# Kernel optimization log

Measured on AMD Instinct MI355X. Metric: run time of the kernel, lower is better.

Reference implementation:

```python
import jax, jax.numpy as jnp
import numpy as np

DMODEL = 1024
NUM_HEADS = 16
HEAD_DIM = DMODEL // NUM_HEADS


def setup_inputs() -> dict:
    key = jax.random.key(0)
    k_x, k_wqkv, k_bqkv, k_wo, k_bo = jax.random.split(key, 5)
    B, T, D = 4, 2048, DMODEL
    s = 1.0 / np.sqrt(D)
    return {
        "x": jax.random.normal(k_x, (B, T, D), dtype=jnp.float32),
        "w_qkv": jax.random.uniform(k_wqkv, (D, 3 * D), dtype=jnp.float32, minval=-s, maxval=s),
        "b_qkv": jax.random.uniform(k_bqkv, (3 * D,), dtype=jnp.float32, minval=-s, maxval=s),
        "w_out": jax.random.uniform(k_wo, (D, D), dtype=jnp.float32, minval=-s, maxval=s),
        "b_out": jax.random.uniform(k_bo, (D,), dtype=jnp.float32, minval=-s, maxval=s),
    }


def reference(x, w_qkv, b_qkv, w_out, b_out):
    B, T, D = x.shape
    H, Hd = NUM_HEADS, HEAD_DIM
    qkv = x @ w_qkv + b_qkv                      # [B,T,3D]
    qkv = qkv.reshape(B, T, 3, H, Hd)
    q = jnp.transpose(qkv[:, :, 0], (0, 2, 1, 3))  # [B,H,T,Hd]
    k = jnp.transpose(qkv[:, :, 1], (0, 2, 1, 3))
    v = jnp.transpose(qkv[:, :, 2], (0, 2, 1, 3))
    scores = jnp.einsum("bhqd,bhkd->bhqk", q, k) / jnp.sqrt(jnp.float32(Hd))
    weights = jax.nn.softmax(scores, axis=-1)
    attn = jnp.einsum("bhqk,bhkd->bhqd", weights, v)  # [B,H,T,Hd]
    attn = jnp.transpose(attn, (0, 2, 1, 3)).reshape(B, T, D)
    return attn @ w_out + b_out
```

## Files before the change

### kernel.cpp

```cpp
#include <hip/hip_runtime.h>
#include <hip/hip_bf16.h>


typedef __bf16 bf16_t;
typedef __bf16 bf16x8 __attribute__((ext_vector_type(8)));
typedef float f32x4 __attribute__((ext_vector_type(4)));
typedef short short4v __attribute__((ext_vector_type(4)));

#if __has_builtin(__builtin_amdgcn_mfma_f32_16x16x16_bf16)
typedef __bf16 bf16x4 __attribute__((ext_vector_type(4)));
#define MFMA_PV(va, vb, c) __builtin_amdgcn_mfma_f32_16x16x16_bf16( \
    __builtin_bit_cast(bf16x4, (va)), __builtin_bit_cast(bf16x4, (vb)), (c), 0, 0, 0)
#else
#define MFMA_PV(va, vb, c) __builtin_amdgcn_mfma_f32_16x16x16bf16_1k((va), (vb), (c), 0, 0, 0)
#endif

#define DMODEL 1024
#define NH     16
#define HD     64
#define BATCH  4
#define SEQ    2048
#define NTOK   (BATCH * SEQ)
#define NOUT   (NTOK * DMODEL)
#define CEXP   0.1803368801111204f

__device__ __forceinline__ void async_ld16(void* lds, const void* g) {
  __builtin_amdgcn_global_load_lds(
      (const __attribute__((address_space(1))) void*)g,
      (__attribute__((address_space(3))) void*)lds, 16, 0, 0);
}

__global__ __launch_bounds__(256) void sniff_dtype(
    const uint4* __restrict__ x, int* __restrict__ flag) {
  int t = threadIdx.x;
  uint4 v = x[t];
  int nanish = 0, zc = 0;
  for (int j = 0; j < 4; ++j) {
    uint4 w = x[t + j * 256];
    unsigned u[4] = {w.x, w.y, w.z, w.w};
    for (int k = 0; k < 4; ++k) {
      unsigned lo = u[k] & 0xFFFFu, hi = u[k] >> 16;
      if ((lo & 0x7F80u) == 0x7F80u) nanish++;
      if ((hi & 0x7F80u) == 0x7F80u) nanish++;
      if (lo == 0) zc++;
      if (hi == 0) zc++;
    }
  }
  (void)v;
  __shared__ int rn[256], rz[256];
  rn[t] = nanish; rz[t] = zc;
  __syncthreads();
  for (int s = 128; s > 0; s >>= 1) {
    if (t < s) { rn[t] += rn[t + s]; rz[t] += rz[t + s]; }
    __syncthreads();
  }
  if (t == 0) flag[0] = (rn[0] > 4 || rz[0] > 2048) ? 1 : 0;
}

__global__ __launch_bounds__(256) void conv_to_bf16(
    const void* __restrict__ src, bf16_t* __restrict__ dst, int n,
    const int* __restrict__ flag) {
  int i = (blockIdx.x * 256 + threadIdx.x) * 8;
  if (i >= n) return;
  if (flag[0]) {
    const float4* s = (const float4*)((const float*)src + i);
    float4 a = s[0], b = s[1];
    bf16_t* o = dst + i;
    o[0] = (bf16_t)a.x; o[1] = (bf16_t)a.y; o[2] = (bf16_t)a.z; o[3] = (bf16_t)a.w;
    o[4] = (bf16_t)b.x; o[5] = (bf16_t)b.y; o[6] = (bf16_t)b.z; o[7] = (bf16_t)b.w;
  } else {
    *(uint4*)(dst + i) = *(const uint4*)((const bf16_t*)src + i);
  }
}

__global__ __launch_bounds__(256) void conv_biases(
    const void* __restrict__ sq, const void* __restrict__ so,
    float* __restrict__ dq, float* __restrict__ dofs,
    const int* __restrict__ flag) {
  int i = blockIdx.x * 256 + threadIdx.x;
  if (i < 3072)
    dq[i] = flag[0] ? ((const float*)sq)[i] : (float)((const bf16_t*)sq)[i];
  else {
    int j = i - 3072;
    dofs[j] = flag[0] ? ((const float*)so)[j] : (float)((const bf16_t*)so)[j];
  }
}

__global__ __launch_bounds__(256) void transpose_w(
    const void* __restrict__ in, bf16_t* __restrict__ out, int R, int C,
    const int* __restrict__ flag) {
  __shared__ bf16_t tile[32][33];
  const int tx = threadIdx.x & 31, ty = threadIdx.x >> 5;
  const int c0 = blockIdx.x * 32, r0 = blockIdx.y * 32;
  if (flag[0]) {
    for (int i = 0; i < 4; ++i) {
      int r = ty + i * 8;
      tile[r][tx] = (bf16_t)((const float*)in)[(size_t)(r0 + r) * C + c0 + tx];
    }
  } else {
    for (int i = 0; i < 4; ++i) {
      int r = ty + i * 8;
      tile[r][tx] = ((const bf16_t*)in)[(size_t)(r0 + r) * C + c0 + tx];
    }
  }
  __syncthreads();
  for (int i = 0; i < 4; ++i) {
    int r = ty + i * 8;
    out[(size_t)(c0 + r) * R + r0 + tx] = tile[tx][r];
  }
}

template <int MODE>
__global__ __launch_bounds__(256) void gemm_bt_bias(
    const bf16_t* __restrict__ A, const bf16_t* __restrict__ Bt,
    const float* __restrict__ bias, void* __restrict__ Cout,
    int M, int N, int K, const int* __restrict__ flag,
    bf16_t* __restrict__ vT) {
  __shared__ bf16_t sA[2][128 * 32];
  __shared__ bf16_t sB[2][128 * 32];
  const int t = threadIdx.x;
  const int wave = t >> 6, lane = t & 63;
  const int quad = lane >> 4, l16 = lane & 15;
  const int nwg = gridDim.x * gridDim.y;
  const int lin = blockIdx.y * gridDim.x + blockIdx.x;
  const int cpx = nwg >> 3;
  const int swz = (lin & 7) * cpx + (lin >> 3);
  const int bx = swz % gridDim.x, by = swz / gridDim.x;
  const int bM = by * 128, bN = bx * 128;
  const int m0w = (wave >> 1) * 64, n0w = (wave & 1) * 64;
  const int rowS = wave * 16 + (lane >> 2);
  const int kcS = (lane & 3) * 8;

  f32x4 acc[4][4] = {};

  auto stage = [&](int buf, int k0) {
    for (int r = 0; r < 2; ++r) {
      int row = r * 64 + rowS;
      async_ld16((char*)sA[buf] + r * 4096 + wave * 1024,
                 A + (size_t)(bM + row) * K + k0 + kcS);
      async_ld16((char*)sB[buf] + r * 4096 + wave * 1024,
                 Bt + (size_t)(bN + row) * K + k0 + kcS);
    }
  };

  const int nsteps = K >> 5;
  stage(0, 0);

  for (int s = 0; s < nsteps; ++s) {
    const int cur = s & 1;
    if (s + 1 < nsteps) {
      stage(cur ^ 1, (s + 1) << 5);
      asm volatile("s_waitcnt vmcnt(4)" ::: "memory");
    } else {
      asm volatile("s_waitcnt vmcnt(0)" ::: "memory");
    }
    __builtin_amdgcn_s_barrier();
    asm volatile("" ::: "memory");

    bf16x8 af[4], bfr[4];
    for (int i = 0; i < 4; ++i)
      af[i] = *(const bf16x8*)&sA[cur][(m0w + i * 16 + l16) * 32 + quad * 8];
    for (int j = 0; j < 4; ++j)
      bfr[j] = *(const bf16x8*)&sB[cur][(n0w + j * 16 + l16) * 32 + quad * 8];
    for (int i = 0; i < 4; ++i)
      for (int j = 0; j < 4; ++j)
        acc[i][j] = __builtin_amdgcn_mfma_f32_16x16x32_bf16(af[i], bfr[j], acc[i][j], 0, 0, 0);

    asm volatile("" ::: "memory");
    __builtin_amdgcn_s_barrier();
  }

  const bool f32out = (MODE == 1) && flag[0];
  for (int j = 0; j < 4; ++j) {
    int col = bN + n0w + j * 16 + l16;
    float bv = bias[col];
    for (int i = 0; i < 4; ++i) {
      int row0 = bM + m0w + i * 16 + quad * 4;
      if (MODE == 2 && col >= 2048) {
        int hh = (col - 2048) >> 6, dd = (col - 2048) & 63;
        bf16_t o4[4];
        for (int r = 0; r < 4; ++r) o4[r] = (bf16_t)(acc[i][j][r] + bv);
        size_t dst = ((((size_t)(row0 >> 11) * NH + hh) * HD + dd) << 11) | (row0 & 2047);
        *(uint2*)&vT[dst] = *(uint2*)o4;
      } else {
        float scale = (MODE == 2 && col < 1024) ? CEXP : 1.0f;
        for (int r = 0; r < 4; ++r) {
          float v = (acc[i][j][r] + bv) * scale;
          if (f32out) ((float*)Cout)[(size_t)(row0 + r) * N + col] = v;
          else        ((bf16_t*)Cout)[(size_t)(row0 + r) * N + col] = (bf16_t)v;
        }
      }
    }
  }
}

__global__ __launch_bounds__(512) void attention_v9(
    const bf16_t* __restrict__ qkv, const bf16_t* __restrict__ vT,
    bf16_t* __restrict__ attn) {
  const int t = threadIdx.x;
  const int wave = t >> 6, lane = t & 63;
  const int quad = lane >> 4, l16 = lane & 15;
  const int bh = blockIdx.x, b = bh >> 4, h = bh & 15;
  const int qw = blockIdx.y * 256 + wave * 32;

  __shared__ bf16_t Kt[2][128 * 64];
  __shared__ bf16_t Vt[2][64 * 128];

  const bf16_t* qglob = qkv + (size_t)b * SEQ * 3072 + h * 64;
  const bf16_t* kglob = qglob + 1024;
  const bf16_t* vglob = vT + (size_t)bh * HD * SEQ;

  bf16x8 qf[2][2];
  for (int s = 0; s < 2; ++s) {
    const bf16_t* qrow = qglob + (size_t)(qw + s * 16 + l16) * 3072 + quad * 8;
    qf[s][0] = *(const bf16x8*)qrow;
    qf[s][1] = *(const bf16x8*)(qrow + 32);
  }

  f32x4 accO[2][4] = {};
  f32x4 lp[2] = {};

  const int kRow = lane >> 3, kSlot = lane & 7;
  const int vRow = lane >> 4, vSlot = lane & 15;

  auto stageKV = [&](int buf, int kt) {
    for (int j = 0; j < 2; ++j) {
      int keyl = wave * 16 + j * 8 + kRow;
      int gc = kSlot ^ (keyl & 7);
      async_ld16((char*)Kt[buf] + (wave * 16 + j * 8) * 128,
                 kglob + (size_t)(kt + keyl) * 3072 + gc * 8);
    }
    for (int j = 0; j < 2; ++j) {
      int d = wave * 8 + j * 4 + vRow;
      int gc = vSlot ^ (d & 15);
      async_ld16((char*)Vt[buf] + (wave * 8 + j * 4) * 256,
                 vglob + (size_t)d * SEQ + kt + gc * 8);
    }
  };

  stageKV(0, 0);

  for (int ti = 0; ti < SEQ / 128; ++ti) {
    const int buf = ti & 1;
    __syncthreads();
    if (ti + 1 < SEQ / 128) stageKV(buf ^ 1, (ti + 1) * 128);

    const bf16_t* KtB = Kt[buf];
    const bf16_t* VtB = Vt[buf];

    for (int kb = 0; kb < 8; ++kb) {
      const bf16_t* kr = &KtB[(kb * 16 + l16) * 64];
      bf16x8 kf0 = *(const bf16x8*)(kr + ((quad ^ (l16 & 7)) * 8));
      bf16x8 kf1 = *(const bf16x8*)(kr + (((4 + quad) ^ (l16 & 7)) * 8));

      short4v pB[2];
      for (int s = 0; s < 2; ++s) {
        f32x4 z = {0.f, 0.f, 0.f, 0.f};
        f32x4 st = __builtin_amdgcn_mfma_f32_16x16x32_bf16(kf0, qf[s][0], z, 0, 0, 0);
        st = __builtin_amdgcn_mfma_f32_16x16x32_bf16(kf1, qf[s][1], st, 0, 0, 0);
        union { bf16_t hh[4]; short4v s4; } u;
        for (int r = 0; r < 4; ++r) {
          float p = __builtin_amdgcn_exp2f(st[r]);
          lp[s][r] += p;
          u.hh[r] = (bf16_t)p;
        }
        pB[s] = u.s4;
      }

      const int chunkbase = kb * 2 + (quad >> 1);
      const int coff = (quad & 1) * 4;
      for (int db = 0; db < 4; ++db) {
        short4v vf = *(const short4v*)&VtB[(db * 16 + l16) * 128 +
                                           ((chunkbase ^ l16) * 8) + coff];
        for (int s = 0; s < 2; ++s)
          accO[s][db] = MFMA_PV(vf, pB[s], accO[s][db]);
      }
    }
  }

  for (int s = 0; s < 2; ++s) {
    float l = (lp[s][0] + lp[s][1]) + (lp[s][2] + lp[s][3]);
    l += __shfl_xor(l, 16);
    l += __shfl_xor(l, 32);
    float inv = 1.f / l;
    size_t tok = (size_t)b * SEQ + qw + s * 16 + l16;
    for (int db = 0; db < 4; ++db) {
      bf16_t o4[4];
      for (int r = 0; r < 4; ++r) o4[r] = (bf16_t)(accO[s][db][r] * inv);
      *(uint2*)&attn[tok * DMODEL + h * HD + db * 16 + quad * 4] = *(uint2*)o4;
    }
  }
}

extern "C" void kernel_launch(void* const* d_in, const int* in_sizes, int n_in,
                              void* d_out, int out_size, void* d_ws, size_t ws_size,
                              hipStream_t stream) {
  const void* x     = d_in[0];
  const void* w_qkv = d_in[1];
  const void* b_qkv = d_in[2];
  const void* w_out = d_in[3];
  const void* b_out = d_in[4];

  char* ws = (char*)d_ws;
  int*    flag  = (int*)ws;
  bf16_t* wqkvT = (bf16_t*)(ws + 4096);
  bf16_t* woutT = (bf16_t*)(ws + 6295552);
  float*  bqkvf = (float*)(ws + 8392704);
  float*  boutf = (float*)(ws + 8404992);
  bf16_t* qkv   = (bf16_t*)(ws + 8409088);
  bf16_t* xb    = (bf16_t*)(ws + 58740736);
  bf16_t* attn  = xb;
  bf16_t* vTbuf = (bf16_t*)(ws + 75517952);

  sniff_dtype<<<1, 256, 0, stream>>>((const uint4*)x, flag);

  conv_to_bf16<<<NOUT / 2048, 256, 0, stream>>>(x, xb, NOUT, flag);
  conv_biases<<<16, 256, 0, stream>>>(b_qkv, b_out, bqkvf, boutf, flag);

  transpose_w<<<dim3(96, 32), 256, 0, stream>>>(w_qkv, wqkvT, 1024, 3072, flag);
  transpose_w<<<dim3(32, 32), 256, 0, stream>>>(w_out, woutT, 1024, 1024, flag);

  gemm_bt_bias<2><<<dim3(24, 64), 256, 0, stream>>>(
      xb, wqkvT, bqkvf, qkv, NTOK, 3072, 1024, flag, vTbuf);

  attention_v9<<<dim3(BATCH * NH, SEQ / 256), 512, 0, stream>>>(qkv, vTbuf, attn);

  gemm_bt_bias<1><<<dim3(8, 64), 256, 0, stream>>>(
      attn, woutT, boutf, d_out, NTOK, 1024, 1024, flag, nullptr);
}
```

Before: 302.2 us.

## Add 256x256-tile QKV GEMM kernel with swizzled LDS and interleaved staging

Replaces the 128x128 QKV projection GEMM with a new 512-thread kernel computing 256x256 tiles over K steps of 64. Each K step is split into halves whose async loads are interleaved with MFMA groups, with LDS offsets XOR-swizzled and wave priority raised around compute phases. The larger tile raises arithmetic intensity and cuts global traffic, at the cost of 128KB of LDS per block, so only one block fits per CU, and fewer blocks overall. The attention kernel also switches its softmax denominator from a per-register vector accumulator to a scalar sum.

Result: no change. 297.0 us (-1.7%).

```diff
diff --git a/kernel.cpp b/kernel.cpp
--- a/kernel.cpp
+++ b/kernel.cpp
@@ -114,8 +114,7 @@
 __global__ __launch_bounds__(256) void gemm_bt_bias(
     const bf16_t* __restrict__ A, const bf16_t* __restrict__ Bt,
     const float* __restrict__ bias, void* __restrict__ Cout,
-    int M, int N, int K, const int* __restrict__ flag,
-    bf16_t* __restrict__ vT) {
+    int M, int N, int K, const int* __restrict__ flag) {
   __shared__ bf16_t sA[2][128 * 32];
   __shared__ bf16_t sB[2][128 * 32];
   const int t = threadIdx.x;
@@ -176,22 +175,142 @@
     float bv = bias[col];
     for (int i = 0; i < 4; ++i) {
       int row0 = bM + m0w + i * 16 + quad * 4;
-      if (MODE == 2 && col >= 2048) {
+      for (int r = 0; r < 4; ++r) {
+        float v = acc[i][j][r] + bv;
+        if (f32out) ((float*)Cout)[(size_t)(row0 + r) * N + col] = v;
+        else        ((bf16_t*)Cout)[(size_t)(row0 + r) * N + col] = (bf16_t)v;
+      }
+    }
+  }
+}
+
+__global__ __launch_bounds__(512) void gemm256_qkv(
+    const bf16_t* __restrict__ A, const bf16_t* __restrict__ Bt,
+    const float* __restrict__ bias, bf16_t* __restrict__ Cout,
+    int M, int N, int K, bf16_t* __restrict__ vT) {
+  __shared__ __align__(16) char smem[131072];
+  char* lds = smem;
+  const int t = threadIdx.x;
+  const int wave = t >> 6, lane = t & 63;
+  const int quad = lane >> 4, l16 = lane & 15;
+  const int wr = wave >> 2, wc = wave & 3;
+  const int nwg = gridDim.x * gridDim.y;
+  const int lin = blockIdx.y * gridDim.x + blockIdx.x;
+  const int cpx = nwg >> 3;
+  const int swzb = (lin & 7) * cpx + (lin >> 3);
+  const int bx = swzb % gridDim.x, by = swzb / gridDim.x;
+  const int bM = by * 256, bN = bx * 256;
+
+  const int srow = t >> 2;
+  const int xr = ((srow >> 3) & 1) | (((srow >> 2) & 1) << 1);
+  const int skl = ((t ^ xr) & 3) * 8;
+  const size_t offA0 = (size_t)(bM + srow) * K + skl;
+  const size_t offB0 = (size_t)(bN + srow) * K + skl;
+  const size_t off1 = (size_t)128 * K;
+  const int ldsw = wave * 1024;
+
+#define STG_A(bufo, h, k0t) do {                                               \
+    async_ld16(lds + (bufo) + (h) * 16384 + ldsw, A + offA0 + (k0t) + (h) * 32);\
+    async_ld16(lds + (bufo) + (h) * 16384 + 8192 + ldsw,                       \
+               A + offA0 + off1 + (k0t) + (h) * 32); } while (0)
+#define STG_B(bufo, h, k0t) do {                                               \
+    async_ld16(lds + (bufo) + 32768 + (h) * 16384 + ldsw,                      \
+               Bt + offB0 + (k0t) + (h) * 32);                                 \
+    async_ld16(lds + (bufo) + 32768 + (h) * 16384 + 8192 + ldsw,               \
+               Bt + offB0 + off1 + (k0t) + (h) * 32); } while (0)
+
+  int aoff[8], boff[4];
+#pragma unroll
+  for (int mf = 0; mf < 8; ++mf) {
+    int r = wr * 128 + mf * 16 + l16;
+    aoff[mf] = ((r << 6) + (quad << 4)) ^ (((r & 8) << 1) | ((r & 4) << 3));
+  }
+#pragma unroll
+  for (int nf = 0; nf < 4; ++nf) {
+    int r = wc * 64 + nf * 16 + l16;
+    boff[nf] = 32768 + (((r << 6) + (quad << 4)) ^ (((r & 8) << 1) | ((r & 4) << 3)));
+  }
+
+  f32x4 acc[8][4] = {};
+  bf16x8 af[4], bf[4];
+
+#define LDA_SET(mfb, h, bufo) do {                                             \
+    af[0] = *(const bf16x8*)(lds + (bufo) + (h) * 16384 + aoff[(mfb) + 0]);    \
+    af[1] = *(const bf16x8*)(lds + (bufo) + (h) * 16384 + aoff[(mfb) + 1]);    \
+    af[2] = *(const bf16x8*)(lds + (bufo) + (h) * 16384 + aoff[(mfb) + 2]);    \
+    af[3] = *(const bf16x8*)(lds + (bufo) + (h) * 16384 + aoff[(mfb) + 3]); } while (0)
+#define LDB_SET(h, bufo) do {                                                  \
+    bf[0] = *(const bf16x8*)(lds + (bufo) + (h) * 16384 + boff[0]);            \
+    bf[1] = *(const bf16x8*)(lds + (bufo) + (h) * 16384 + boff[1]);            \
+    bf[2] = *(const bf16x8*)(lds + (bufo) + (h) * 16384 + boff[2]);            \
+    bf[3] = *(const bf16x8*)(lds + (bufo) + (h) * 16384 + boff[3]); } while (0)
+#define MFMA16(mfb) do {                                                       \
+    _Pragma("unroll") for (int i_ = 0; i_ < 4; ++i_)                           \
+      { _Pragma("unroll") for (int j_ = 0; j_ < 4; ++j_)                       \
+        acc[(mfb) + i_][j_] = __builtin_amdgcn_mfma_f32_16x16x32_bf16(         \
+            af[i_], bf[j_], acc[(mfb) + i_][j_], 0, 0, 0); } } while (0)
+#define BAR1() do { __builtin_amdgcn_s_barrier(); asm volatile("" ::: "memory"); \
+    __builtin_amdgcn_s_setprio(1); } while (0)
+#define BAR2() do { __builtin_amdgcn_s_setprio(0);                             \
+    asm volatile("" ::: "memory"); __builtin_amdgcn_s_barrier(); } while (0)
+
+  const int NT = K >> 6;
+  STG_A(0, 0, 0); STG_B(0, 0, 0); STG_A(0, 1, 0); STG_B(0, 1, 0);
+  STG_A(65536, 0, 64); STG_B(65536, 0, 64);
+  asm volatile("s_waitcnt vmcnt(4)" ::: "memory");
+  __builtin_amdgcn_s_barrier();
+  asm volatile("" ::: "memory");
+
+  for (int T = 0; T < NT; ++T) {
+    const int bufo = (T & 1) << 16;
+    const int obufo = bufo ^ 65536;
+    const int k1 = (T + 1) << 6, k2 = (T + 2) << 6;
+    LDA_SET(0, 0, bufo); LDB_SET(0, bufo);
+    if (T + 1 < NT) STG_A(obufo, 1, k1);
+    BAR1(); MFMA16(0); BAR2();
+    LDA_SET(4, 0, bufo);
+    if (T + 1 < NT) STG_B(obufo, 1, k1);
+    BAR1(); MFMA16(4); BAR2();
+    LDA_SET(0, 1, bufo); LDB_SET(1, bufo);
+    if (T + 2 < NT) STG_A(bufo, 0, k2);
+    BAR1(); MFMA16(0); BAR2();
+    LDA_SET(4, 1, bufo);
+    if (T + 2 < NT) {
+      STG_B(bufo, 0, k2);
+      asm volatile("s_waitcnt vmcnt(4)" ::: "memory");
+    } else {
+      asm volatile("s_waitcnt vmcnt(0)" ::: "memory");
+    }
+    BAR1(); MFMA16(4); BAR2();
+  }
+
+#pragma unroll
+  for (int nf = 0; nf < 4; ++nf) {
+    int col = bN + wc * 64 + nf * 16 + l16;
+    float bv = bias[col];
+#pragma unroll
+    for (int mf = 0; mf < 8; ++mf) {
+      int row0 = bM + wr * 128 + mf * 16 + quad * 4;
+      if (col >= 2048) {
         int hh = (col - 2048) >> 6, dd = (col - 2048) & 63;
         bf16_t o4[4];
-        for (int r = 0; r < 4; ++r) o4[r] = (bf16_t)(acc[i][j][r] + bv);
+        for (int r = 0; r < 4; ++r) o4[r] = (bf16_t)(acc[mf][nf][r] + bv);
         size_t dst = ((((size_t)(row0 >> 11) * NH + hh) * HD + dd) << 11) | (row0 & 2047);
         *(uint2*)&vT[dst] = *(uint2*)o4;
       } else {
-        float scale = (MODE == 2 && col < 1024) ? CEXP : 1.0f;
-        for (int r = 0; r < 4; ++r) {
-          float v = (acc[i][j][r] + bv) * scale;
-          if (f32out) ((float*)Cout)[(size_t)(row0 + r) * N + col] = v;
-          else        ((bf16_t*)Cout)[(size_t)(row0 + r) * N + col] = (bf16_t)v;
-        }
+        float scale = (col < 1024) ? CEXP : 1.0f;
+        for (int r = 0; r < 4; ++r)
+          Cout[(size_t)(row0 + r) * N + col] = (bf16_t)((acc[mf][nf][r] + bv) * scale);
       }
     }
   }
+#undef STG_A
+#undef STG_B
+#undef LDA_SET
+#undef LDB_SET
+#undef MFMA16
+#undef BAR1
+#undef BAR2
 }
 
 __global__ __launch_bounds__(512) void attention_v9(
@@ -218,7 +337,7 @@
   }
 
   f32x4 accO[2][4] = {};
-  f32x4 lp[2] = {};
+  float lpart[2] = {0.f, 0.f};
 
   const int kRow = lane >> 3, kSlot = lane & 7;
   const int vRow = lane >> 4, vSlot = lane & 15;
@@ -261,7 +380,7 @@
         union { bf16_t hh[4]; short4v s4; } u;
         for (int r = 0; r < 4; ++r) {
           float p = __builtin_amdgcn_exp2f(st[r]);
-          lp[s][r] += p;
+          lpart[s] += p;
           u.hh[r] = (bf16_t)p;
         }
         pB[s] = u.s4;
@@ -279,7 +398,7 @@
   }
 
   for (int s = 0; s < 2; ++s) {
-    float l = (lp[s][0] + lp[s][1]) + (lp[s][2] + lp[s][3]);
+    float l = lpart[s];
     l += __shfl_xor(l, 16);
     l += __shfl_xor(l, 32);
     float inv = 1.f / l;
@@ -320,11 +439,11 @@
   transpose_w<<<dim3(96, 32), 256, 0, stream>>>(w_qkv, wqkvT, 1024, 3072, flag);
   transpose_w<<<dim3(32, 32), 256, 0, stream>>>(w_out, woutT, 1024, 1024, flag);
 
-  gemm_bt_bias<2><<<dim3(24, 64), 256, 0, stream>>>(
-      xb, wqkvT, bqkvf, qkv, NTOK, 3072, 1024, flag, vTbuf);
+  gemm256_qkv<<<dim3(12, 32), 512, 0, stream>>>(
+      xb, wqkvT, bqkvf, qkv, NTOK, 3072, 1024, vTbuf);
 
   attention_v9<<<dim3(BATCH * NH, SEQ / 256), 512, 0, stream>>>(qkv, vTbuf, attn);
 
   gemm_bt_bias<1><<<dim3(8, 64), 256, 0, stream>>>(
-      attn, woutT, boutf, d_out, NTOK, 1024, 1024, flag, nullptr);
-}
+      attn, woutT, boutf, d_out, NTOK, 1024, 1024, flag);
+}
```
